# Kernel optimization log

Measured on AMD Instinct MI355X. Metric: run time of the kernel, lower is better.

## Reference

```python
import jax, jax.numpy as jnp
import numpy as np

K, D = 512, 64


def setup_inputs() -> dict:
    key = jax.random.key(0)
    k1, k2 = jax.random.split(key)
    z_e_x = jax.random.normal(k1, (32, 4096, D), dtype=jnp.float32)
    # nn.Embedding weight initialized uniform(-1/K, 1/K)
    codebook = jax.random.uniform(k2, (K, D), dtype=jnp.float32,
                                  minval=-1.0 / K, maxval=1.0 / K)
    return {"z_e_x": z_e_x, "codebook": codebook}


def reference(z_e_x, codebook):
    # vq(): pairwise squared L2 distances to codebook, then argmin.
    d = z_e_x.shape[-1]
    flat = z_e_x.reshape(-1, d)                                   # [N, D]
    # ||z||^2 - 2 z.e + ||e||^2  (addmm form from original vq)
    dists = (jnp.sum(flat * flat, axis=1, keepdims=True)
             - 2.0 * flat @ codebook.T
             + jnp.sum(codebook * codebook, axis=1))              # [N, K]
    indices = jnp.argmin(dists, axis=1)                            # [N]
    # latents: indices reshaped to input shape minus feature dim
    return indices.reshape(z_e_x.shape[:-1])
```

## Files before the change

### kernel.cpp

```cpp
#include <hip/hip_runtime.h>
#include <math.h>

#define K_CODES 512
#define D_DIM   64
#define BM      512
#define THREADS 512
#define LSTR    72
#define EPS_GAP 4e-5f

#define WS_CNT_OFF  2048
#define WS_EH_OFF   4096
#define WS_EL_OFF   77824
#define WS_LIST_OFF 151552

typedef __attribute__((ext_vector_type(8))) short short8v;
typedef __attribute__((ext_vector_type(4))) float f32x4;

__device__ __forceinline__ float np_sumsq64(const float* zarr) {
    float L[16];
#pragma unroll
    for (int j = 0; j < 16; ++j)
        L[j] = __fadd_rn(
            __fadd_rn(__fmul_rn(zarr[j],      zarr[j]),
                      __fmul_rn(zarr[j + 16], zarr[j + 16])),
            __fadd_rn(__fmul_rn(zarr[j + 32], zarr[j + 32]),
                      __fmul_rn(zarr[j + 48], zarr[j + 48])));
    float m[8];
#pragma unroll
    for (int j = 0; j < 8; ++j) m[j] = __fadd_rn(L[j], L[j + 8]);
    float n4[4];
#pragma unroll
    for (int j = 0; j < 4; ++j) n4[j] = __fadd_rn(m[j], m[j + 4]);
    return __fadd_rn(__fadd_rn(n4[0], n4[2]), __fadd_rn(n4[1], n4[3]));
}

__device__ __forceinline__ unsigned short f32_bf16_rne(float x) {
    unsigned int u = __float_as_uint(x);
    unsigned int r = (u + 0x7FFFu + ((u >> 16) & 1u)) >> 16;
    return (unsigned short)r;
}
__device__ __forceinline__ float bf16_f32(unsigned short h) {
    return __uint_as_float(((unsigned int)h) << 16);
}
__device__ __forceinline__ void split2(float x, unsigned short& h, unsigned short& l) {
    h = f32_bf16_rne(x);
    l = f32_bf16_rne(x - bf16_f32(h));
}

__global__ __launch_bounds__(256)
void vq_prep_kernel(const float* __restrict__ cb, float* __restrict__ ws,
                    int do_split) {
    int g = blockIdx.x * blockDim.x + threadIdx.x;
    if (g == 0) *reinterpret_cast<int*>((char*)ws + WS_CNT_OFF) = 0;
    int k = g >> 2, q = g & 3;
    if (k >= K_CODES) return;
    const float* row = cb + (size_t)k * D_DIM;
    if (q == 0) {
        float e[D_DIM];
        const float4* p = reinterpret_cast<const float4*>(row);
#pragma unroll
        for (int i = 0; i < 16; ++i) {
            float4 v = p[i];
            e[4*i+0]=v.x; e[4*i+1]=v.y; e[4*i+2]=v.z; e[4*i+3]=v.w;
        }
        ws[k] = np_sumsq64(e);
    }
    if (do_split) {
        unsigned short* eh = reinterpret_cast<unsigned short*>((char*)ws + WS_EH_OFF)
                             + (size_t)k * LSTR;
        unsigned short* el = reinterpret_cast<unsigned short*>((char*)ws + WS_EL_OFF)
                             + (size_t)k * LSTR;
#pragma unroll
        for (int i = 16 * q; i < 16 * q + 16; ++i) {
            unsigned short h, l;
            split2(row[i], h, l);
            eh[i] = h; el[i] = l;
        }
        if (q == 3)
#pragma unroll
            for (int i = D_DIM; i < LSTR; ++i) { eh[i] = 0; el[i] = 0; }
    }
}

__global__ __launch_bounds__(512)
void vq_pass1_mono(const float* __restrict__ z,
                   const unsigned short* __restrict__ eh_g,
                   const unsigned short* __restrict__ el_g,
                   const float* __restrict__ norms, int* __restrict__ out,
                   int* __restrict__ cnt, int* __restrict__ list, int cap, int n) {
    __shared__ __align__(16) unsigned short ehS[K_CODES * LSTR];
    __shared__ __align__(16) unsigned short elS[K_CODES * LSTR];
    __shared__ __align__(16) float nrmS[K_CODES];

    const int tid  = threadIdx.x;
    const int l    = tid & 63;
    const int w    = tid >> 6;
    const int j    = l >> 4;
    const int c16  = l & 15;
    const int base = blockIdx.x * BM;

    {
        const char* esrc = (const char*)eh_g;
        const char* lsrc = (const char*)el_g;
#pragma unroll
        for (int r = 0; r < 9; ++r) {
            size_t off = ((size_t)tid + (size_t)r * THREADS) * 16;
            __builtin_amdgcn_global_load_lds(
                (const __attribute__((address_space(1))) void*)(esrc + off),
                (__attribute__((address_space(3))) void*)((char*)ehS + off), 16, 0, 0);
            __builtin_amdgcn_global_load_lds(
                (const __attribute__((address_space(1))) void*)(lsrc + off),
                (__attribute__((address_space(3))) void*)((char*)elS + off), 16, 0, 0);
        }
        if (tid < K_CODES / 4)
            reinterpret_cast<float4*>(nrmS)[tid] =
                reinterpret_cast<const float4*>(norms)[tid];
    }

    short8v bzh[4][2], bzl[4][2];
#pragma unroll
    for (int p = 0; p < 4; ++p) {
        int row = base + (4 * w + p) * 16 + c16;
        if (row >= n) row = n - 1;
        const float* zp = z + (size_t)row * D_DIM + j * 8;
#pragma unroll
        for (int h = 0; h < 2; ++h) {
            float4 v0 = *reinterpret_cast<const float4*>(zp + h * 32);
            float4 v1 = *reinterpret_cast<const float4*>(zp + h * 32 + 4);
            unsigned short hh[8], ll[8];
            split2(v0.x, hh[0], ll[0]); split2(v0.y, hh[1], ll[1]);
            split2(v0.z, hh[2], ll[2]); split2(v0.w, hh[3], ll[3]);
            split2(v1.x, hh[4], ll[4]); split2(v1.y, hh[5], ll[5]);
            split2(v1.z, hh[6], ll[6]); split2(v1.w, hh[7], ll[7]);
            short8v th, tl;
#pragma unroll
            for (int i = 0; i < 8; ++i) { th[i] = (short)hh[i]; tl[i] = (short)ll[i]; }
            bzh[p][h] = th; bzl[p][h] = tl;
        }
    }

    __syncthreads();

    float m1[4] = {INFINITY, INFINITY, INFINITY, INFINITY};
    float m2[4] = {INFINITY, INFINITY, INFINITY, INFINITY};
    int   i1[4] = {0, 0, 0, 0};

#pragma unroll 4
    for (int ct = 0; ct < 32; ++ct) {
        int ar = (ct * 16 + c16) * LSTR + j * 8;
        short8v aeh0 = *reinterpret_cast<const short8v*>(&ehS[ar]);
        short8v aeh1 = *reinterpret_cast<const short8v*>(&ehS[ar + 32]);
        short8v ael0 = *reinterpret_cast<const short8v*>(&elS[ar]);
        short8v ael1 = *reinterpret_cast<const short8v*>(&elS[ar + 32]);
        float4 nr = *reinterpret_cast<const float4*>(&nrmS[ct * 16 + j * 4]);
        float nra[4] = {nr.x, nr.y, nr.z, nr.w};
        int kg0 = ct * 16 + j * 4;
#pragma unroll
        for (int p = 0; p < 4; ++p) {
            f32x4 acc = {0.f, 0.f, 0.f, 0.f};
            acc = __builtin_amdgcn_mfma_f32_16x16x32_bf16(aeh0, bzh[p][0], acc, 0, 0, 0);
            acc = __builtin_amdgcn_mfma_f32_16x16x32_bf16(aeh1, bzh[p][1], acc, 0, 0, 0);
            acc = __builtin_amdgcn_mfma_f32_16x16x32_bf16(aeh0, bzl[p][0], acc, 0, 0, 0);
            acc = __builtin_amdgcn_mfma_f32_16x16x32_bf16(aeh1, bzl[p][1], acc, 0, 0, 0);
            acc = __builtin_amdgcn_mfma_f32_16x16x32_bf16(ael0, bzh[p][0], acc, 0, 0, 0);
            acc = __builtin_amdgcn_mfma_f32_16x16x32_bf16(ael1, bzh[p][1], acc, 0, 0, 0);
#pragma unroll
            for (int r = 0; r < 4; ++r) {
                float s = fmaf(-2.0f, acc[r], nra[r]);
                int kg = kg0 + r;
                bool lt1 = s < m1[p];
                float nm2 = lt1 ? m1[p] : fminf(s, m2[p]);
                i1[p] = lt1 ? kg : i1[p];
                m1[p] = lt1 ? s : m1[p];
                m2[p] = nm2;
            }
        }
    }

#pragma unroll
    for (int p = 0; p < 4; ++p) {
        float a1 = m1[p], a2 = m2[p]; int ai = i1[p];
#pragma unroll
        for (int off = 16; off <= 32; off <<= 1) {
            float o1 = __shfl_xor(a1, off, 64);
            float o2 = __shfl_xor(a2, off, 64);
            int   oi = __shfl_xor(ai, off, 64);
            float hi = fmaxf(a1, o1);
            bool take = o1 < a1;
            ai = take ? oi : ai;
            a1 = take ? o1 : a1;
            a2 = fminf(hi, fminf(a2, o2));
        }
        int  ptg    = base + (4 * w + p) * 16 + c16;
        bool writer = (j == 0) && (ptg < n);
        bool flag   = writer && (a2 - a1 <= EPS_GAP);
        unsigned long long m = __ballot(flag);
        int abase = 0;
        if (m) {
            int leader = __ffsll(m) - 1;
            if (l == leader) abase = atomicAdd(cnt, __popcll(m));
            abase = __shfl(abase, leader, 64);
        }
        if (writer) {
            int val = ai;
            if (flag) {
                int rank = __popcll(m & ((1ull << l) - 1ull));
                int slot = abase + rank;
                if (slot < cap) list[slot] = ptg;
                else            val |= (int)0x80000000;
            }
            out[ptg] = val;
        }
    }
}

__global__ __launch_bounds__(256)
void vq_pass1_legacy(const float* __restrict__ z, const float* __restrict__ cb,
                     const float* __restrict__ norms, int* __restrict__ out,
                     int* __restrict__ cnt, int* __restrict__ list, int cap, int n) {
    __shared__ unsigned short zhS[128 * LSTR];
    __shared__ unsigned short zlS[128 * LSTR];
    __shared__ unsigned short ehS[128 * LSTR];
    __shared__ unsigned short elS[128 * LSTR];
    __shared__ float nrmL[128];

    const int tid  = threadIdx.x;
    const int l    = tid & 63;
    const int w    = tid >> 6;
    const int j    = l >> 4;
    const int c16  = l & 15;
    const int base = blockIdx.x * 128;

    const float4* z4 = reinterpret_cast<const float4*>(z);
#pragma unroll
    for (int rep = 0; rep < 8; ++rep) {
        int flat = rep * 256 + tid;
        int pt   = flat >> 4;
        int dblk = flat & 15;
        int gp = base + pt; if (gp >= n) gp = n - 1;
        float4 v = z4[(size_t)gp * 16 + dblk];
        ushort4 h, lo;
        split2(v.x, h.x, lo.x); split2(v.y, h.y, lo.y);
        split2(v.z, h.z, lo.z); split2(v.w, h.w, lo.w);
        *reinterpret_cast<ushort4*>(&zhS[pt * LSTR + dblk * 4]) = h;
        *reinterpret_cast<ushort4*>(&zlS[pt * LSTR + dblk * 4]) = lo;
    }
    __syncthreads();

    short8v bzh[2][2], bzl[2][2];
#pragma unroll
    for (int p = 0; p < 2; ++p) {
        int pr = ((2 * w + p) * 16 + c16) * LSTR;
#pragma unroll
        for (int h = 0; h < 2; ++h) {
            int off = pr + h * 32 + j * 8;
            bzh[p][h] = *reinterpret_cast<const short8v*>(&zhS[off]);
            bzl[p][h] = *reinterpret_cast<const short8v*>(&zlS[off]);
        }
    }

    float m1[2] = {INFINITY, INFINITY};
    float m2[2] = {INFINITY, INFINITY};
    int   i1[2] = {0, 0};

    for (int c = 0; c < 4; ++c) {
        __syncthreads();
        const float4* cb4 = reinterpret_cast<const float4*>(cb);
#pragma unroll
        for (int rep = 0; rep < 8; ++rep) {
            int flat = rep * 256 + tid;
            int code = flat >> 4;
            int dblk = flat & 15;
            float4 v = cb4[(size_t)(c * 128 + code) * 16 + dblk];
            ushort4 h, lo;
            split2(v.x, h.x, lo.x); split2(v.y, h.y, lo.y);
            split2(v.z, h.z, lo.z); split2(v.w, h.w, lo.w);
            *reinterpret_cast<ushort4*>(&ehS[code * LSTR + dblk * 4]) = h;
            *reinterpret_cast<ushort4*>(&elS[code * LSTR + dblk * 4]) = lo;
        }
        if (tid < 32)
            reinterpret_cast<float4*>(nrmL)[tid] =
                reinterpret_cast<const float4*>(norms)[c * 32 + tid];
        __syncthreads();

#pragma unroll
        for (int ct = 0; ct < 8; ++ct) {
            int ar = (ct * 16 + c16) * LSTR + j * 8;
            short8v aeh0 = *reinterpret_cast<const short8v*>(&ehS[ar]);
            short8v aeh1 = *reinterpret_cast<const short8v*>(&ehS[ar + 32]);
            short8v ael0 = *reinterpret_cast<const short8v*>(&elS[ar]);
            short8v ael1 = *reinterpret_cast<const short8v*>(&elS[ar + 32]);
            float4 nr = *reinterpret_cast<const float4*>(&nrmL[ct * 16 + j * 4]);
            float nra[4] = {nr.x, nr.y, nr.z, nr.w};
            int kg0 = c * 128 + ct * 16 + j * 4;
#pragma unroll
            for (int p = 0; p < 2; ++p) {
                f32x4 acc = {0.f, 0.f, 0.f, 0.f};
                acc = __builtin_amdgcn_mfma_f32_16x16x32_bf16(aeh0, bzh[p][0], acc, 0, 0, 0);
                acc = __builtin_amdgcn_mfma_f32_16x16x32_bf16(aeh1, bzh[p][1], acc, 0, 0, 0);
                acc = __builtin_amdgcn_mfma_f32_16x16x32_bf16(aeh0, bzl[p][0], acc, 0, 0, 0);
                acc = __builtin_amdgcn_mfma_f32_16x16x32_bf16(aeh1, bzl[p][1], acc, 0, 0, 0);
                acc = __builtin_amdgcn_mfma_f32_16x16x32_bf16(ael0, bzh[p][0], acc, 0, 0, 0);
                acc = __builtin_amdgcn_mfma_f32_16x16x32_bf16(ael1, bzh[p][1], acc, 0, 0, 0);
#pragma unroll
                for (int r = 0; r < 4; ++r) {
                    float s = fmaf(-2.0f, acc[r], nra[r]);
                    int kg = kg0 + r;
                    bool lt1 = s < m1[p];
                    float nm2 = lt1 ? m1[p] : fminf(s, m2[p]);
                    i1[p] = lt1 ? kg : i1[p];
                    m1[p] = lt1 ? s : m1[p];
                    m2[p] = nm2;
                }
            }
        }
    }

#pragma unroll
    for (int p = 0; p < 2; ++p) {
        float a1 = m1[p], a2 = m2[p]; int ai = i1[p];
#pragma unroll
        for (int off = 16; off <= 32; off <<= 1) {
            float o1 = __shfl_xor(a1, off, 64);
            float o2 = __shfl_xor(a2, off, 64);
            int   oi = __shfl_xor(ai, off, 64);
            float hi = fmaxf(a1, o1);
            bool take = o1 < a1;
            ai = take ? oi : ai;
            a1 = take ? o1 : a1;
            a2 = fminf(hi, fminf(a2, o2));
        }
        int  ptg    = base + (2 * w + p) * 16 + c16;
        bool writer = (j == 0) && (ptg < n);
        bool flag   = writer && (a2 - a1 <= EPS_GAP);
        unsigned long long m = __ballot(flag);
        int abase = 0;
        if (m) {
            int leader = __ffsll(m) - 1;
            if (l == leader) abase = atomicAdd(cnt, __popcll(m));
            abase = __shfl(abase, leader, 64);
        }
        if (writer) {
            int val = ai;
            if (flag) {
                int rank = __popcll(m & ((1ull << l) - 1ull));
                int slot = abase + rank;
                if (slot < cap) list[slot] = ptg;
                else            val |= (int)0x80000000;
            }
            out[ptg] = val;
        }
    }
}

__global__ __launch_bounds__(256)
void vq_cleanup_kernel(const float* __restrict__ z, const float* __restrict__ cb,
                       const float* __restrict__ norms,
                       const int* __restrict__ cnt, const int* __restrict__ list,
                       int cap, int* __restrict__ out, int n) {
    __shared__ float rbv[4];
    __shared__ int   rbi[4];
    const int tid  = threadIdx.x;
    const int lane = tid & 63;
    const int wv   = tid >> 6;

    int total = *cnt;
    int lim   = total < cap ? total : cap;

    for (int i = blockIdx.x; i < lim; i += gridDim.x) {
        int pt = list[i];
        float zr[D_DIM];
        const float4* zp = reinterpret_cast<const float4*>(z + (size_t)pt * D_DIM);
#pragma unroll
        for (int g = 0; g < 16; ++g) {
            float4 q = zp[g];
            zr[4*g+0]=q.x; zr[4*g+1]=q.y; zr[4*g+2]=q.z; zr[4*g+3]=q.w;
        }
        const float sz = np_sumsq64(zr);
        float best = INFINITY; int bi = 0x7FFFFFFF;
#pragma unroll 1
        for (int r = 0; r < 2; ++r) {
            int k = tid * 2 + r;
            const float4* e4 = reinterpret_cast<const float4*>(cb) + ((size_t)k << 4);
            float a = 0.f;
#pragma unroll
            for (int g = 0; g < 16; ++g) {
                float4 q = e4[g];
                a = fmaf(zr[4*g+0], q.x, a);
                a = fmaf(zr[4*g+1], q.y, a);
                a = fmaf(zr[4*g+2], q.z, a);
                a = fmaf(zr[4*g+3], q.w, a);
            }
            float s = __fadd_rn(__fsub_rn(sz, __fmul_rn(2.0f, a)), norms[k]);
            if (s < best || (s == best && k < bi)) { best = s; bi = k; }
        }
#pragma unroll
        for (int off = 1; off < 64; off <<= 1) {
            float os = __shfl_xor(best, off, 64);
            int   ok = __shfl_xor(bi, off, 64);
            if (os < best || (os == best && ok < bi)) { best = os; bi = ok; }
        }
        if (lane == 0) { rbv[wv] = best; rbi[wv] = bi; }
        __syncthreads();
        if (tid == 0) {
            float b = rbv[0]; int id = rbi[0];
#pragma unroll
            for (int q = 1; q < 4; ++q) {
                float v = rbv[q]; int vi = rbi[q];
                if (v < b || (v == b && vi < id)) { b = v; id = vi; }
            }
            out[pt] = id;
        }
        __syncthreads();
    }

    if (total > cap) {
        const int wid    = (blockIdx.x * blockDim.x + tid) >> 6;
        const int nwaves = (gridDim.x * blockDim.x) >> 6;
        for (int b = wid * 64; b < n; b += nwaves * 64) {
            int t = b + lane;
            int v = (t < n) ? out[t] : 0;
            unsigned long long m = __ballot(v < 0);
            while (m) {
                int bb = __ffsll(m) - 1;
                m &= m - 1ull;
                int pt = b + bb;
                float zr[D_DIM];
                const float4* zp = reinterpret_cast<const float4*>(z + (size_t)pt * D_DIM);
#pragma unroll
                for (int g = 0; g < 16; ++g) {
                    float4 q = zp[g];
                    zr[4*g+0]=q.x; zr[4*g+1]=q.y; zr[4*g+2]=q.z; zr[4*g+3]=q.w;
                }
                const float sz = np_sumsq64(zr);
                float best = INFINITY; int bi = 0x7FFFFFFF;
#pragma unroll 1
                for (int r = 0; r < 8; ++r) {
                    const float4* e4 = reinterpret_cast<const float4*>(cb) +
                                       ((size_t)(lane * 8 + r) << 4);
                    float a = 0.f;
#pragma unroll
                    for (int g = 0; g < 16; ++g) {
                        float4 q = e4[g];
                        a = fmaf(zr[4*g+0], q.x, a);
                        a = fmaf(zr[4*g+1], q.y, a);
                        a = fmaf(zr[4*g+2], q.z, a);
                        a = fmaf(zr[4*g+3], q.w, a);
                    }
                    float s = __fadd_rn(__fsub_rn(sz, __fmul_rn(2.0f, a)),
                                        norms[lane * 8 + r]);
                    if (s < best) { best = s; bi = lane * 8 + r; }
                }
#pragma unroll
                for (int off = 1; off < 64; off <<= 1) {
                    float os = __shfl_xor(best, off, 64);
                    int   ok = __shfl_xor(bi, off, 64);
                    if (os < best || (os == best && ok < bi)) { best = os; bi = ok; }
                }
                if (lane == 0) out[pt] = bi;
            }
        }
    }
}

extern "C" void kernel_launch(void* const* d_in, const int* in_sizes, int n_in,
                              void* d_out, int out_size, void* d_ws, size_t ws_size,
                              hipStream_t stream) {
    const float* z  = (const float*)d_in[0];
    const float* cb = (const float*)d_in[1];
    int n = in_sizes[0] / D_DIM;
    float* norms = (float*)d_ws;
    int*   cnt   = (int*)((char*)d_ws + WS_CNT_OFF);
    int* out = (int*)d_out;

    bool fast = ws_size >= (size_t)WS_LIST_OFF + 4096;
    vq_prep_kernel<<<(4 * K_CODES + 255) / 256, 256, 0, stream>>>(cb, norms, fast ? 1 : 0);

    if (fast) {
        const unsigned short* eh = (const unsigned short*)((char*)d_ws + WS_EH_OFF);
        const unsigned short* el = (const unsigned short*)((char*)d_ws + WS_EL_OFF);
        int* list = (int*)((char*)d_ws + WS_LIST_OFF);
        int  cap  = (int)((ws_size - WS_LIST_OFF) / 4);
        vq_pass1_mono<<<(n + BM - 1) / BM, THREADS, 0, stream>>>(
            z, eh, el, norms, out, cnt, list, cap, n);
        vq_cleanup_kernel<<<2048, 256, 0, stream>>>(z, cb, norms, cnt, list, cap, out, n);
    } else {
        int* list = (int*)d_ws + 513;
        int  cap  = (int)(ws_size / 4) - 513; if (cap < 0) cap = 0;
        vq_pass1_legacy<<<(n + 127) / 128, 256, 0, stream>>>(
            z, cb, norms, out, cnt, list, cap, n);
        vq_cleanup_kernel<<<2048, 256, 0, stream>>>(z, cb, norms, cnt, list, cap, out, n);
    }
}
```

Baseline: 61.00 us.

## Pack code index into distance bits, fold norm into MFMA init, stage codebook in LDS

```diff
diff --git a/kernel.cpp b/kernel.cpp
--- a/kernel.cpp
+++ b/kernel.cpp
@@ -6,7 +6,8 @@
 #define BM      512
 #define THREADS 512
 #define LSTR    72
-#define EPS_GAP 4e-5f
+#define CLS     65
+#define EPS_GAP 6e-5f
 
 #define WS_CNT_OFF  2048
 #define WS_EH_OFF   4096
@@ -97,6 +98,7 @@
     const int w    = tid >> 6;
     const int j    = l >> 4;
     const int c16  = l & 15;
+    const int j4   = j * 4;
     const int base = blockIdx.x * BM;
 
     {
@@ -128,10 +130,10 @@
             float4 v0 = *reinterpret_cast<const float4*>(zp + h * 32);
             float4 v1 = *reinterpret_cast<const float4*>(zp + h * 32 + 4);
             unsigned short hh[8], ll[8];
-            split2(v0.x, hh[0], ll[0]); split2(v0.y, hh[1], ll[1]);
-            split2(v0.z, hh[2], ll[2]); split2(v0.w, hh[3], ll[3]);
-            split2(v1.x, hh[4], ll[4]); split2(v1.y, hh[5], ll[5]);
-            split2(v1.z, hh[6], ll[6]); split2(v1.w, hh[7], ll[7]);
+            split2(-2.0f * v0.x, hh[0], ll[0]); split2(-2.0f * v0.y, hh[1], ll[1]);
+            split2(-2.0f * v0.z, hh[2], ll[2]); split2(-2.0f * v0.w, hh[3], ll[3]);
+            split2(-2.0f * v1.x, hh[4], ll[4]); split2(-2.0f * v1.y, hh[5], ll[5]);
+            split2(-2.0f * v1.z, hh[6], ll[6]); split2(-2.0f * v1.w, hh[7], ll[7]);
             short8v th, tl;
 #pragma unroll
             for (int i = 0; i < 8; ++i) { th[i] = (short)hh[i]; tl[i] = (short)ll[i]; }
@@ -143,53 +145,56 @@
 
     float m1[4] = {INFINITY, INFINITY, INFINITY, INFINITY};
     float m2[4] = {INFINITY, INFINITY, INFINITY, INFINITY};
-    int   i1[4] = {0, 0, 0, 0};
 
 #pragma unroll 4
-    for (int ct = 0; ct < 32; ++ct) {
+    for (int cti = 0; cti < 32; ++cti) {
+        const int ct = (cti + 4 * w) & 31;
         int ar = (ct * 16 + c16) * LSTR + j * 8;
         short8v aeh0 = *reinterpret_cast<const short8v*>(&ehS[ar]);
         short8v aeh1 = *reinterpret_cast<const short8v*>(&ehS[ar + 32]);
         short8v ael0 = *reinterpret_cast<const short8v*>(&elS[ar]);
         short8v ael1 = *reinterpret_cast<const short8v*>(&elS[ar + 32]);
-        float4 nr = *reinterpret_cast<const float4*>(&nrmS[ct * 16 + j * 4]);
-        float nra[4] = {nr.x, nr.y, nr.z, nr.w};
-        int kg0 = ct * 16 + j * 4;
+        float4 nr = *reinterpret_cast<const float4*>(&nrmS[ct * 16 + j4]);
+        f32x4 nrv = {nr.x, nr.y, nr.z, nr.w};
+
+        f32x4 acc[4];
+#pragma unroll
+        for (int p = 0; p < 4; ++p) acc[p] = nrv;
+        __builtin_amdgcn_s_setprio(1);
 #pragma unroll
         for (int p = 0; p < 4; ++p) {
-            f32x4 acc = {0.f, 0.f, 0.f, 0.f};
-            acc = __builtin_amdgcn_mfma_f32_16x16x32_bf16(aeh0, bzh[p][0], acc, 0, 0, 0);
-            acc = __builtin_amdgcn_mfma_f32_16x16x32_bf16(aeh1, bzh[p][1], acc, 0, 0, 0);
-            acc = __builtin_amdgcn_mfma_f32_16x16x32_bf16(aeh0, bzl[p][0], acc, 0, 0, 0);
-            acc = __builtin_amdgcn_mfma_f32_16x16x32_bf16(aeh1, bzl[p][1], acc, 0, 0, 0);
-            acc = __builtin_amdgcn_mfma_f32_16x16x32_bf16(ael0, bzh[p][0], acc, 0, 0, 0);
-            acc = __builtin_amdgcn_mfma_f32_16x16x32_bf16(ael1, bzh[p][1], acc, 0, 0, 0);
+            acc[p] = __builtin_amdgcn_mfma_f32_16x16x32_bf16(aeh0, bzh[p][0], acc[p], 0, 0, 0);
+            acc[p] = __builtin_amdgcn_mfma_f32_16x16x32_bf16(aeh1, bzh[p][1], acc[p], 0, 0, 0);
+            acc[p] = __builtin_amdgcn_mfma_f32_16x16x32_bf16(aeh0, bzl[p][0], acc[p], 0, 0, 0);
+            acc[p] = __builtin_amdgcn_mfma_f32_16x16x32_bf16(aeh1, bzl[p][1], acc[p], 0, 0, 0);
+            acc[p] = __builtin_amdgcn_mfma_f32_16x16x32_bf16(ael0, bzh[p][0], acc[p], 0, 0, 0);
+            acc[p] = __builtin_amdgcn_mfma_f32_16x16x32_bf16(ael1, bzh[p][1], acc[p], 0, 0, 0);
+        }
+        __builtin_amdgcn_s_setprio(0);
+
+        const unsigned kb = (unsigned)(ct * 16) | (unsigned)j4;
+#pragma unroll
+        for (int p = 0; p < 4; ++p) {
 #pragma unroll
             for (int r = 0; r < 4; ++r) {
-                float s = fmaf(-2.0f, acc[r], nra[r]);
-                int kg = kg0 + r;
-                bool lt1 = s < m1[p];
-                float nm2 = lt1 ? m1[p] : fminf(s, m2[p]);
-                i1[p] = lt1 ? kg : i1[p];
-                m1[p] = lt1 ? s : m1[p];
-                m2[p] = nm2;
+                unsigned bits = (__float_as_uint(acc[p][r]) & 0xFFFFFE00u)
+                                | (kb + (unsigned)r);
+                float pk = __uint_as_float(bits);
+                m2[p] = fminf(m2[p], fmaxf(m1[p], pk));
+                m1[p] = fminf(m1[p], pk);
             }
         }
     }
 
 #pragma unroll
     for (int p = 0; p < 4; ++p) {
-        float a1 = m1[p], a2 = m2[p]; int ai = i1[p];
+        float a1 = m1[p], a2 = m2[p];
 #pragma unroll
         for (int off = 16; off <= 32; off <<= 1) {
             float o1 = __shfl_xor(a1, off, 64);
             float o2 = __shfl_xor(a2, off, 64);
-            int   oi = __shfl_xor(ai, off, 64);
-            float hi = fmaxf(a1, o1);
-            bool take = o1 < a1;
-            ai = take ? oi : ai;
-            a1 = take ? o1 : a1;
-            a2 = fminf(hi, fminf(a2, o2));
+            a2 = fminf(fminf(a2, o2), fmaxf(a1, o1));
+            a1 = fminf(a1, o1);
         }
         int  ptg    = base + (4 * w + p) * 16 + c16;
         bool writer = (j == 0) && (ptg < n);
@@ -202,7 +207,7 @@
             abase = __shfl(abase, leader, 64);
         }
         if (writer) {
-            int val = ai;
+            int val = (int)(__float_as_uint(a1) & 0x1FFu);
             if (flag) {
                 int rank = __popcll(m & ((1ull << l) - 1ull));
                 int slot = abase + rank;
@@ -358,12 +363,24 @@
                        const float* __restrict__ norms,
                        const int* __restrict__ cnt, const int* __restrict__ list,
                        int cap, int* __restrict__ out, int n) {
+    __shared__ float cbS[K_CODES * CLS];
     __shared__ float rbv[4];
     __shared__ int   rbi[4];
     const int tid  = threadIdx.x;
     const int lane = tid & 63;
     const int wv   = tid >> 6;
 
+    {
+        const float4* cb4 = reinterpret_cast<const float4*>(cb);
+        for (int i = tid; i < K_CODES * 16; i += 256) {
+            float4 v = cb4[i];
+            int row = i >> 4, col = (i & 15) * 4;
+            float* d = &cbS[row * CLS + col];
+            d[0] = v.x; d[1] = v.y; d[2] = v.z; d[3] = v.w;
+        }
+    }
+    __syncthreads();
+
     int total = *cnt;
     int lim   = total < cap ? total : cap;
 
@@ -379,18 +396,13 @@
         const float sz = np_sumsq64(zr);
         float best = INFINITY; int bi = 0x7FFFFFFF;
 #pragma unroll 1
-        for (int r = 0; r < 2; ++r) {
-            int k = tid * 2 + r;
-            const float4* e4 = reinterpret_cast<const float4*>(cb) + ((size_t)k << 4);
+        for (int rr = 0; rr < 2; ++rr) {
+            int k = tid + rr * 256;
+            const float* e = &cbS[k * CLS];
             float a = 0.f;
 #pragma unroll
-            for (int g = 0; g < 16; ++g) {
-                float4 q = e4[g];
-                a = fmaf(zr[4*g+0], q.x, a);
-                a = fmaf(zr[4*g+1], q.y, a);
-                a = fmaf(zr[4*g+2], q.z, a);
-                a = fmaf(zr[4*g+3], q.w, a);
-            }
+            for (int d = 0; d < D_DIM; ++d)
+                a = fmaf(zr[d], e[d], a);
             float s = __fadd_rn(__fsub_rn(sz, __fmul_rn(2.0f, a)), norms[k]);
             if (s < best || (s == best && k < bi)) { best = s; bi = k; }
         }
@@ -436,20 +448,14 @@
                 float best = INFINITY; int bi = 0x7FFFFFFF;
 #pragma unroll 1
                 for (int r = 0; r < 8; ++r) {
-                    const float4* e4 = reinterpret_cast<const float4*>(cb) +
-                                       ((size_t)(lane * 8 + r) << 4);
+                    int k = lane * 8 + r;
+                    const float* e = &cbS[k * CLS];
                     float a = 0.f;
 #pragma unroll
-                    for (int g = 0; g < 16; ++g) {
-                        float4 q = e4[g];
-                        a = fmaf(zr[4*g+0], q.x, a);
-                        a = fmaf(zr[4*g+1], q.y, a);
-                        a = fmaf(zr[4*g+2], q.z, a);
-                        a = fmaf(zr[4*g+3], q.w, a);
-                    }
-                    float s = __fadd_rn(__fsub_rn(sz, __fmul_rn(2.0f, a)),
-                                        norms[lane * 8 + r]);
-                    if (s < best) { best = s; bi = lane * 8 + r; }
+                    for (int d = 0; d < D_DIM; ++d)
+                        a = fmaf(zr[d], e[d], a);
+                    float s = __fadd_rn(__fsub_rn(sz, __fmul_rn(2.0f, a)), norms[k]);
+                    if (s < best) { best = s; bi = k; }
                 }
 #pragma unroll
                 for (int off = 1; off < 64; off <<= 1) {
@@ -483,12 +489,12 @@
         int  cap  = (int)((ws_size - WS_LIST_OFF) / 4);
         vq_pass1_mono<<<(n + BM - 1) / BM, THREADS, 0, stream>>>(
             z, eh, el, norms, out, cnt, list, cap, n);
-        vq_cleanup_kernel<<<2048, 256, 0, stream>>>(z, cb, norms, cnt, list, cap, out, n);
+        vq_cleanup_kernel<<<256, 256, 0, stream>>>(z, cb, norms, cnt, list, cap, out, n);
     } else {
         int* list = (int*)d_ws + 513;
         int  cap  = (int)(ws_size / 4) - 513; if (cap < 0) cap = 0;
         vq_pass1_legacy<<<(n + 127) / 128, 256, 0, stream>>>(
             z, cb, norms, out, cnt, list, cap, n);
-        vq_cleanup_kernel<<<2048, 256, 0, stream>>>(z, cb, norms, cnt, list, cap, out, n);
-    }
-}
+        vq_cleanup_kernel<<<256, 256, 0, stream>>>(z, cb, norms, cnt, list, cap, out, n);
+    }
+}
```

Result: slower. 63.77 us (+4.5%).
